# Kernel tuning notes

Measured on AMD Instinct MI355X. Metric: run time of the kernel, lower is better.

## Reference

```python
import jax, jax.numpy as jnp
import numpy as np

N = 4096           # batch size (square similarity matrix)
NUM_BINS = 10      # histogram bins (module default)
NUM_CLASSES = 64   # classes used to synthesize the relevance matrix


def setup_inputs() -> dict:
    key = jax.random.key(0)
    k1, k2 = jax.random.split(key)
    # cosine similarities in [-1, 1]
    batch = jax.random.uniform(k1, (N, N), jnp.float32, -1.0, 1.0)
    # relevance matrix from class labels: labels[i,j] = 1 if same class
    cls = jax.random.randint(k2, (N,), 0, NUM_CLASSES)
    labels = (cls[:, None] == cls[None, :]).astype(jnp.float32)
    return {"batch": batch, "labels": labels}


def reference(batch, labels):
    num_bins = NUM_BINS
    I_pos = labels
    I_neg = 1.0 - labels
    N_pos = jnp.sum(labels, axis=1)                      # [N]
    dist2 = 2.0 - 2.0 * jnp.clip(batch, -1.0, 1.0)       # [N, N], in [0, 4]
    Delta = 4.0 / num_bins
    Z = jnp.linspace(0.0, 4.0, num_bins + 1)             # [L], L = num_bins+1

    # soft binning pulse for all bins at once: [N, N, L]
    pulse = jnp.maximum(0.0, 1.0 - jnp.abs(dist2[..., None] - Z) / Delta)
    h_pos = jnp.einsum('nml,nm->nl', pulse, I_pos)       # [N, L]
    h_neg = jnp.einsum('nml,nm->nl', pulse, I_neg)       # [N, L]

    H_pos = jnp.cumsum(h_pos, axis=1)
    H = jnp.cumsum(h_pos + h_neg, axis=1)

    # FastAP = h_pos * H_pos / H, with nan/inf (H == 0) set to 0
    safe_H = jnp.where(H > 0, H, 1.0)
    ap_terms = jnp.where(H > 0, h_pos * H_pos / safe_H, 0.0)

    safe_Np = jnp.where(N_pos > 0, N_pos, 1.0)
    ap = jnp.sum(ap_terms, axis=1) / safe_Np             # [N]

    # drop NaN rows (N_pos == 0) from the mean, matching FastAP[~isnan]
    valid = N_pos > 0
    mean_ap = jnp.sum(jnp.where(valid, ap, 0.0)) / jnp.sum(valid.astype(ap.dtype))
    return 1.0 - mean_ap
```

## Files before the change

kernel.cpp:

```cpp
#include <hip/hip_runtime.h>

#define N 4096
#define NUM_BINS 10
#define L (NUM_BINS + 1)
#define SLOTS (2 * L + 1)
#define BLOCK 256

__global__ __launch_bounds__(BLOCK) void fastap_row_kernel(
    const float* __restrict__ batch, const float* __restrict__ labels,
    float* __restrict__ ap_out, float* __restrict__ valid_out)
{
    __shared__ float hist[SLOTS][BLOCK];

    const int tid = threadIdx.x;
    const int row = blockIdx.x;

    #pragma unroll
    for (int s = 0; s < SLOTS - 1; ++s) hist[s][tid] = 0.f;

    const float4* b4 = (const float4*)(batch + (size_t)row * N);
    const float4* l4 = (const float4*)(labels + (size_t)row * N);

    float npos = 0.f;
    #pragma unroll
    for (int it = 0; it < N / (4 * BLOCK); ++it) {
        float4 bv = b4[it * BLOCK + tid];
        float4 lv = l4[it * BLOCK + tid];
        #pragma unroll
        for (int e = 0; e < 4; ++e) {
            float x   = ((const float*)&bv)[e];
            float lbl = ((const float*)&lv)[e];
            x = fminf(fmaxf(x, -1.f), 1.f);
            float t = (2.f - 2.f * x) * 2.5f;
            int k = (int)t;
            if (k > NUM_BINS) k = NUM_BINS;
            float frac = t - (float)k;
            int k2 = k + 1;
            if (k2 > NUM_BINS) k2 = NUM_BINS;
            int base = (lbl > 0.5f) ? 0 : L;
            hist[base + k ][tid] += 1.f - frac;
            hist[base + k2][tid] += frac;
            npos += lbl;
        }
    }
    hist[SLOTS - 1][tid] = npos;
    __syncthreads();

    for (int s = BLOCK / 2; s > 0; s >>= 1) {
        if (tid < s) {
            #pragma unroll
            for (int b = 0; b < SLOTS; ++b)
                hist[b][tid] += hist[b][tid + s];
        }
        __syncthreads();
    }

    if (tid == 0) {
        float Hp = 0.f, Hs = 0.f, ap = 0.f;
        #pragma unroll
        for (int l = 0; l < L; ++l) {
            float hp = hist[l][0];
            float hn = hist[L + l][0];
            Hp += hp;
            Hs += hp + hn;
            if (Hs > 0.f) ap += hp * Hp / Hs;
        }
        float Np = hist[SLOTS - 1][0];
        ap_out[row]    = (Np > 0.f) ? ap / Np : 0.f;
        valid_out[row] = (Np > 0.f) ? 1.f : 0.f;
    }
}

__global__ __launch_bounds__(BLOCK) void fastap_reduce_kernel(
    const float* __restrict__ ap, const float* __restrict__ valid,
    float* __restrict__ out)
{
    const int tid = threadIdx.x;
    float s_ap = 0.f, s_v = 0.f;
    for (int i = tid; i < N; i += BLOCK) {
        s_ap += ap[i];
        s_v  += valid[i];
    }
    #pragma unroll
    for (int off = 32; off > 0; off >>= 1) {
        s_ap += __shfl_down(s_ap, off, 64);
        s_v  += __shfl_down(s_v,  off, 64);
    }
    __shared__ float r_ap[BLOCK / 64], r_v[BLOCK / 64];
    const int wave = tid >> 6;
    if ((tid & 63) == 0) { r_ap[wave] = s_ap; r_v[wave] = s_v; }
    __syncthreads();
    if (tid == 0) {
        float ta = 0.f, tv = 0.f;
        #pragma unroll
        for (int w = 0; w < BLOCK / 64; ++w) { ta += r_ap[w]; tv += r_v[w]; }
        out[0] = 1.f - ta / tv;
    }
}

extern "C" void kernel_launch(void* const* d_in, const int* in_sizes, int n_in,
                              void* d_out, int out_size, void* d_ws, size_t ws_size,
                              hipStream_t stream) {
    const float* batch  = (const float*)d_in[0];
    const float* labels = (const float*)d_in[1];
    float* ap    = (float*)d_ws;
    float* valid = ap + N;
    fastap_row_kernel<<<N, BLOCK, 0, stream>>>(batch, labels, ap, valid);
    fastap_reduce_kernel<<<1, BLOCK, 0, stream>>>(ap, valid, (float*)d_out);
}
```

Baseline: 153.3 us.

## Map one wave per row and accumulate histogram bins in registers

```diff
diff --git a/kernel.cpp b/kernel.cpp
--- a/kernel.cpp
+++ b/kernel.cpp
@@ -3,69 +3,65 @@
 #define N 4096
 #define NUM_BINS 10
 #define L (NUM_BINS + 1)
-#define SLOTS (2 * L + 1)
 #define BLOCK 256
+#define WAVES_PER_BLOCK (BLOCK / 64)
+#define F4_PER_ROW (N / 4)
+#define ITERS (F4_PER_ROW / 64)
 
 __global__ __launch_bounds__(BLOCK) void fastap_row_kernel(
     const float* __restrict__ batch, const float* __restrict__ labels,
     float* __restrict__ ap_out, float* __restrict__ valid_out)
 {
-    __shared__ float hist[SLOTS][BLOCK];
+    const int lane = threadIdx.x & 63;
+    const int wave = threadIdx.x >> 6;
+    const int row  = blockIdx.x * WAVES_PER_BLOCK + wave;
 
-    const int tid = threadIdx.x;
-    const int row = blockIdx.x;
-
-    #pragma unroll
-    for (int s = 0; s < SLOTS - 1; ++s) hist[s][tid] = 0.f;
-
-    const float4* b4 = (const float4*)(batch + (size_t)row * N);
+    const float4* b4 = (const float4*)(batch  + (size_t)row * N);
     const float4* l4 = (const float4*)(labels + (size_t)row * N);
 
-    float npos = 0.f;
+    float acc_pos[L];
+    float acc_all[L];
     #pragma unroll
-    for (int it = 0; it < N / (4 * BLOCK); ++it) {
-        float4 bv = b4[it * BLOCK + tid];
-        float4 lv = l4[it * BLOCK + tid];
+    for (int l = 0; l < L; ++l) { acc_pos[l] = 0.f; acc_all[l] = 0.f; }
+
+    #pragma unroll 4
+    for (int it = 0; it < ITERS; ++it) {
+        float4 bv = b4[it * 64 + lane];
+        float4 lv = l4[it * 64 + lane];
         #pragma unroll
         for (int e = 0; e < 4; ++e) {
             float x   = ((const float*)&bv)[e];
             float lbl = ((const float*)&lv)[e];
             x = fminf(fmaxf(x, -1.f), 1.f);
-            float t = (2.f - 2.f * x) * 2.5f;
-            int k = (int)t;
-            if (k > NUM_BINS) k = NUM_BINS;
-            float frac = t - (float)k;
-            int k2 = k + 1;
-            if (k2 > NUM_BINS) k2 = NUM_BINS;
-            int base = (lbl > 0.5f) ? 0 : L;
-            hist[base + k ][tid] += 1.f - frac;
-            hist[base + k2][tid] += frac;
-            npos += lbl;
+            float t = fmaf(-5.f, x, 5.f);
+            #pragma unroll
+            for (int l = 0; l < L; ++l) {
+                float p = fmaxf(0.f, 1.f - fabsf(t - (float)l));
+                acc_pos[l] = fmaf(p, lbl, acc_pos[l]);
+                acc_all[l] += p;
+            }
         }
     }
-    hist[SLOTS - 1][tid] = npos;
-    __syncthreads();
 
-    for (int s = BLOCK / 2; s > 0; s >>= 1) {
-        if (tid < s) {
-            #pragma unroll
-            for (int b = 0; b < SLOTS; ++b)
-                hist[b][tid] += hist[b][tid + s];
+    #pragma unroll
+    for (int l = 0; l < L; ++l) {
+        #pragma unroll
+        for (int off = 1; off < 64; off <<= 1) {
+            acc_pos[l] += __shfl_xor(acc_pos[l], off, 64);
+            acc_all[l] += __shfl_xor(acc_all[l], off, 64);
         }
-        __syncthreads();
     }
 
-    if (tid == 0) {
+    if (lane == 0) {
         float Hp = 0.f, Hs = 0.f, ap = 0.f;
         #pragma unroll
         for (int l = 0; l < L; ++l) {
-            float hp = hist[l][0];
-            float hn = hist[L + l][0];
+            float hp = acc_pos[l];
             Hp += hp;
-            Hs += hp + hn;
+            Hs += acc_all[l];
             if (Hs > 0.f) ap += hp * Hp / Hs;
         }
-        float Np = hist[SLOTS - 1][0];
+        float Np = Hp;
         ap_out[row]    = (Np > 0.f) ? ap / Np : 0.f;
         valid_out[row] = (Np > 0.f) ? 1.f : 0.f;
     }
@@ -105,6 +101,6 @@
     const float* labels = (const float*)d_in[1];
     float* ap    = (float*)d_ws;
     float* valid = ap + N;
-    fastap_row_kernel<<<N, BLOCK, 0, stream>>>(batch, labels, ap, valid);
+    fastap_row_kernel<<<N / WAVES_PER_BLOCK, BLOCK, 0, stream>>>(batch, labels, ap, valid);
     fastap_reduce_kernel<<<1, BLOCK, 0, stream>>>(ap, valid, (float*)d_out);
 }
```

New measurement: 152.8 us. About the same (-0.3%).
